# Performance work log

Measured on AMD Instinct MI355X. Metric: run time of the kernel, lower is better.

The kernel has to match this reference:

```python
import jax, jax.numpy as jnp
import numpy as np

H = 16          # n_heads
MAX_REL = 16    # max_relative_position


def _rel_index(S, max_rel):
    # Shaw-style clipped relative-distance index matrix [S, S]
    r = np.arange(S)
    dist = np.clip(r[None, :] - r[:, None], -max_rel, max_rel) + max_rel
    return jnp.asarray(dist, dtype=jnp.int32)


def setup_inputs() -> dict:
    key = jax.random.key(0)
    ks = jax.random.split(key, 16)
    B, S, D = 2, 1024, 1024
    dh = D // H
    n_rel = 2 * MAX_REL + 1
    f = lambda k, shape, scale: (jax.random.normal(k, shape, dtype=jnp.float32) * scale)
    w_scale = 1.0 / np.sqrt(D)
    return {
        "query": f(ks[0], (B, S, D), 1.0),
        "key": f(ks[1], (B, S, D), 1.0),
        "value": f(ks[2], (B, S, D), 1.0),
        "Wq": f(ks[3], (D, D), w_scale), "bq": jnp.zeros((D,), jnp.float32),
        "Wk": f(ks[4], (D, D), w_scale), "bk": jnp.zeros((D,), jnp.float32),
        "Wv": f(ks[5], (D, D), w_scale), "bv": jnp.zeros((D,), jnp.float32),
        "Wo": f(ks[6], (D, D), w_scale), "bo": jnp.zeros((D,), jnp.float32),
        "rel_k": f(ks[7], (n_rel, dh), 1.0 / np.sqrt(dh)),
        "rel_v": f(ks[8], (n_rel, dh), 1.0 / np.sqrt(dh)),
    }


def reference(query, key, value, Wq, bq, Wk, bk, Wv, bv, Wo, bo, rel_k, rel_v):
    B, Sq, D = query.shape
    Sk = key.shape[1]
    dh = D // H
    scale = jnp.sqrt(jnp.asarray(dh, dtype=query.dtype))

    q = (query @ Wq + bq).reshape(B, Sq, H, dh)   # [B,Sq,H,dh]
    k = (key @ Wk + bk).reshape(B, Sk, H, dh)
    v = (value @ Wv + bv).reshape(B, Sk, H, dh)

    idx = _rel_index(max(Sq, Sk), MAX_REL)        # len_q == len_k path
    rk = rel_k[idx]                                # [Sq,Sk,dh]
    rv = rel_v[idx]                                # [Sq,Sk,dh]

    attn1 = jnp.einsum('bqhd,bkhd->bhqk', q, k)
    attn2 = jnp.einsum('bqhd,qkd->bhqk', q, rk)
    attn = jax.nn.softmax((attn1 + attn2) / scale, axis=-1)  # [B,H,Sq,Sk]

    w1 = jnp.einsum('bhqk,bkhd->bhqd', attn, v)
    w2 = jnp.einsum('bhqk,qkd->bhqd', attn, rv)
    x = (w1 + w2).transpose(0, 2, 1, 3).reshape(B, Sq, D)
    return x @ Wo + bo
```

## Files before the change

kernel.cpp:

```cpp
#include <hip/hip_runtime.h>
#include <math.h>

#define Hh 16
#define DH 64
#define NR 33

typedef short s16x8 __attribute__((ext_vector_type(8)));
typedef float f32x4 __attribute__((ext_vector_type(4)));
typedef __fp16 h16x2 __attribute__((ext_vector_type(2)));

static __device__ __forceinline__ short f2h(float f) {
    _Float16 h = (_Float16)f;
    short s; __builtin_memcpy(&s, &h, 2); return s;
}
static __device__ __forceinline__ unsigned pk2h(float a, float b) {
    h16x2 h = __builtin_amdgcn_cvt_pkrtz(a, b);
    unsigned r; __builtin_memcpy(&r, &h, 4); return r;
}

static __device__ __forceinline__ void mfma16(f32x4& c, const s16x8& a, const s16x8& b) {
    asm("s_nop 3\n\tv_mfma_f32_16x16x32_f16 %0, %1, %2, %0"
        : "+v"(c) : "v"(a), "v"(b));
}
static __device__ __forceinline__ void mfma16_last(f32x4& c, const s16x8& a, const s16x8& b) {
    asm("s_nop 3\n\tv_mfma_f32_16x16x32_f16 %0, %1, %2, %0\n\ts_nop 7\n\ts_nop 7"
        : "+v"(c) : "v"(a), "v"(b));
}
static __device__ __forceinline__ void acc_guard(f32x4& c) {
    asm volatile("s_nop 7\n\ts_nop 7" : "+v"(c));
}

static __device__ __forceinline__ void gld16(const short* g, short* l) {
    __builtin_amdgcn_global_load_lds(
        (const __attribute__((address_space(1))) void*)g,
        (__attribute__((address_space(3))) void*)l, 16, 0, 0);
}

static __device__ __forceinline__ s16x8 lds_frag(const short* base, int row, int kb) {
    return *(const s16x8*)((const char*)base + row * 128 + (kb ^ ((row & 7) << 4)));
}

__global__ __launch_bounds__(256)
void cvt_w(const float* __restrict__ W0, const float* __restrict__ W1,
           const float* __restrict__ W2, const float* __restrict__ W3,
           short* __restrict__ Wt) {
    __shared__ float ts[32][33];
    const int z = blockIdx.z;
    const float* W = (z == 0) ? W0 : (z == 1) ? W1 : (z == 2) ? W2 : W3;
    short* O = Wt + (size_t)z * 1024 * 1024;
    const int n0 = blockIdx.x * 32, k0 = blockIdx.y * 32;
    const int tx = threadIdx.x & 31, ty = threadIdx.x >> 5;
    #pragma unroll
    for (int rr = 0; rr < 4; ++rr)
        ts[ty + 8 * rr][tx] = W[(size_t)(k0 + ty + 8 * rr) * 1024 + n0 + tx];
    __syncthreads();
    #pragma unroll
    for (int rr = 0; rr < 4; ++rr)
        O[(size_t)(n0 + ty + 8 * rr) * 1024 + k0 + tx] = f2h(ts[tx][ty + 8 * rr]);
}

__global__ __launch_bounds__(256)
void gemm_qkv(const float* __restrict__ Aq, const float* __restrict__ Ak,
              const float* __restrict__ Av, const short* __restrict__ Wt,
              const float* __restrict__ bq, const float* __restrict__ bk,
              const float* __restrict__ bv, short* __restrict__ Out) {
    __shared__ __align__(16) short As[64 * 64];
    __shared__ __align__(16) short Bs[128 * 64];
    const int tid = threadIdx.x;
    const int wave = tid >> 6, lane = tid & 63;
    const int g = lane >> 4, r = lane & 15;
    const int wm = wave >> 1, wn = wave & 1;
    const int n0 = blockIdx.x * 128;
    const int by = blockIdx.y;
    const int slab = by >> 5;
    const int m0 = (by & 31) * 64;
    const float* A    = (slab == 0) ? Aq : (slab == 1) ? Ak : Av;
    const float* bias = (slab == 0) ? bq : (slab == 1) ? bk : bv;
    const short* Bg = Wt + (size_t)slab * 1024 * 1024;
    short* Og = Out + (size_t)slab * 2048 * 1024;

    const int ar = tid >> 2, ak = tid & 3;
    const float* ap = A + (size_t)(m0 + ar) * 1024 + ak * 16;
    char* asb = (char*)As + ar * 128;
    const int aswz = (ar & 7) << 4;
    const int ao0 = (ak * 32) ^ aswz, ao1 = (ak * 32 + 16) ^ aswz;

    const short* bp[4]; short* bl[4];
    #pragma unroll
    for (int i = 0; i < 4; ++i) {
        int s = i * 256 + tid;
        int row = s >> 3, sk = s & 7;
        int gb = (sk * 16) ^ ((row & 7) << 4);
        bp[i] = Bg + (size_t)(n0 + row) * 1024 + gb / 2;
        bl[i] = Bs + (size_t)(i * 256 + wave * 64) * 8;
    }

    f32x4 acc[2][4] = {};
    #pragma unroll
    for (int mi = 0; mi < 2; ++mi)
        #pragma unroll
        for (int nj = 0; nj < 4; ++nj)
            asm volatile("s_nop 7" : "+v"(acc[mi][nj]));

    for (int kt = 0; kt < 1024; kt += 64) {
        #pragma unroll
        for (int i = 0; i < 4; ++i) gld16(bp[i] + kt, bl[i]);
        float4 va[4];
        #pragma unroll
        for (int c = 0; c < 4; ++c) va[c] = *(const float4*)(ap + kt + c * 4);
        unsigned pk[8];
        #pragma unroll
        for (int c = 0; c < 4; ++c) {
            pk[2 * c]     = pk2h(va[c].x, va[c].y);
            pk[2 * c + 1] = pk2h(va[c].z, va[c].w);
        }
        *(uint4*)(asb + ao0) = *(const uint4*)&pk[0];
        *(uint4*)(asb + ao1) = *(const uint4*)&pk[4];
        asm volatile("s_waitcnt vmcnt(0)" ::: "memory");
        __syncthreads();
        #pragma unroll
        for (int ks = 0; ks < 2; ++ks) {
            s16x8 af[2], bf[4];
            #pragma unroll
            for (int mi = 0; mi < 2; ++mi)
                af[mi] = lds_frag(As, wm * 32 + mi * 16 + r, ks * 64 + g * 16);
            #pragma unroll
            for (int nj = 0; nj < 4; ++nj)
                bf[nj] = lds_frag(Bs, wn * 64 + nj * 16 + r, ks * 64 + g * 16);
            #pragma unroll
            for (int mi = 0; mi < 2; ++mi)
                #pragma unroll
                for (int nj = 0; nj < 4; ++nj)
                    mfma16(acc[mi][nj], af[mi], bf[nj]);
        }
        __syncthreads();
    }
    #pragma unroll
    for (int nj = 0; nj < 4; ++nj) {
        int col = n0 + wn * 64 + nj * 16 + r;
        float bv_ = bias[col];
        #pragma unroll
        for (int mi = 0; mi < 2; ++mi) {
            acc_guard(acc[mi][nj]);
            #pragma unroll
            for (int j = 0; j < 4; ++j) {
                int row = m0 + wm * 32 + mi * 16 + g * 4 + j;
                Og[(size_t)row * 1024 + col] = f2h(acc[mi][nj][j] + bv_);
            }
        }
    }
}

__global__ __launch_bounds__(256)
void gemm_out(const short* __restrict__ Xg, const short* __restrict__ Bg,
              const float* __restrict__ bo, float* __restrict__ Og) {
    __shared__ __align__(16) short As[64 * 64];
    __shared__ __align__(16) short Bs[128 * 64];
    const int tid = threadIdx.x;
    const int wave = tid >> 6, lane = tid & 63;
    const int g = lane >> 4, r = lane & 15;
    const int wm = wave >> 1, wn = wave & 1;
    const int n0 = blockIdx.x * 128;
    const int m0 = blockIdx.y * 64;

    const short* xp[2]; short* xl[2];
    #pragma unroll
    for (int i = 0; i < 2; ++i) {
        int s = i * 256 + tid;
        int row = s >> 3, sk = s & 7;
        int gb = (sk * 16) ^ ((row & 7) << 4);
        xp[i] = Xg + (size_t)(m0 + row) * 1024 + gb / 2;
        xl[i] = As + (size_t)(i * 256 + wave * 64) * 8;
    }
    const short* bp[4]; short* bl[4];
    #pragma unroll
    for (int i = 0; i < 4; ++i) {
        int s = i * 256 + tid;
        int row = s >> 3, sk = s & 7;
        int gb = (sk * 16) ^ ((row & 7) << 4);
        bp[i] = Bg + (size_t)(n0 + row) * 1024 + gb / 2;
        bl[i] = Bs + (size_t)(i * 256 + wave * 64) * 8;
    }

    f32x4 acc[2][4] = {};
    #pragma unroll
    for (int mi = 0; mi < 2; ++mi)
        #pragma unroll
        for (int nj = 0; nj < 4; ++nj)
            asm volatile("s_nop 7" : "+v"(acc[mi][nj]));

    for (int kt = 0; kt < 1024; kt += 64) {
        #pragma unroll
        for (int i = 0; i < 2; ++i) gld16(xp[i] + kt, xl[i]);
        #pragma unroll
        for (int i = 0; i < 4; ++i) gld16(bp[i] + kt, bl[i]);
        asm volatile("s_waitcnt vmcnt(0)" ::: "memory");
        __syncthreads();
        #pragma unroll
        for (int ks = 0; ks < 2; ++ks) {
            s16x8 af[2], bf[4];
            #pragma unroll
            for (int mi = 0; mi < 2; ++mi)
                af[mi] = lds_frag(As, wm * 32 + mi * 16 + r, ks * 64 + g * 16);
            #pragma unroll
            for (int nj = 0; nj < 4; ++nj)
                bf[nj] = lds_frag(Bs, wn * 64 + nj * 16 + r, ks * 64 + g * 16);
            #pragma unroll
            for (int mi = 0; mi < 2; ++mi)
                #pragma unroll
                for (int nj = 0; nj < 4; ++nj)
                    mfma16(acc[mi][nj], af[mi], bf[nj]);
        }
        __syncthreads();
    }
    #pragma unroll
    for (int nj = 0; nj < 4; ++nj) {
        int col = n0 + wn * 64 + nj * 16 + r;
        float bv_ = bo[col];
        #pragma unroll
        for (int mi = 0; mi < 2; ++mi) {
            acc_guard(acc[mi][nj]);
            #pragma unroll
            for (int j = 0; j < 4; ++j) {
                int row = m0 + wm * 32 + mi * 16 + g * 4 + j;
                Og[(size_t)row * 1024 + col] = acc[mi][nj][j] + bv_;
            }
        }
    }
}

#define KSTR 72
#define QRSTR 49
#define RVSTR 68

__global__ __launch_bounds__(256)
void attn_mfma(const short* __restrict__ qg, const short* __restrict__ kg,
               const short* __restrict__ vg, const float* __restrict__ relk,
               const float* __restrict__ relv, short* __restrict__ xg) {
    __shared__ __align__(16) short k_s[64 * KSTR];
    __shared__ __align__(16) short vt_s[64 * KSTR];
    __shared__ __align__(16) short p_s[4][16 * KSTR];
    __shared__ float qr_s[64 * QRSTR];
    __shared__ float W_s[64 * NR];
    __shared__ __align__(16) unsigned char relbuf[NR * RVSTR * 4];

    short* rel_h = (short*)relbuf;
    float* rv_s  = (float*)relbuf;

    const int S = 1024, Dm = 1024;
    const int tid = threadIdx.x;
    const int wave = tid >> 6;
    const int lane = tid & 63;
    const int g = lane >> 4;
    const int r = lane & 15;

    const int blk = blockIdx.x;
    const int bh = blk & 31;
    const int qb = blk >> 5;
    const int b = bh >> 4, h = bh & 15;
    const size_t base = (size_t)b * S * Dm + h * DH;
    const int qw = qb * 64 + wave * 16;

    for (int idx = tid; idx < 48 * 64; idx += 256) {
        int row = idx >> 6, col = idx & 63;
        float val = (row < NR) ? relk[row * 64 + col] : 0.f;
        rel_h[row * KSTR + col] = f2h(val);
    }
    for (int idx = tid; idx < 64 * NR; idx += 256) W_s[idx] = 0.f;
    __syncthreads();

    s16x8 qf[2];
    qf[0] = *(const s16x8*)(qg + base + (size_t)(qw + r) * Dm + g * 8);
    qf[1] = *(const s16x8*)(qg + base + (size_t)(qw + r) * Dm + 32 + g * 8);

    #pragma unroll
    for (int ct = 0; ct < 3; ++ct) {
        f32x4 c = {0.f, 0.f, 0.f, 0.f};
        s16x8 bf0 = *(const s16x8*)&rel_h[(ct * 16 + r) * KSTR + g * 8];
        s16x8 bf1 = *(const s16x8*)&rel_h[(ct * 16 + r) * KSTR + 32 + g * 8];
        mfma16(c, qf[0], bf0);
        mfma16_last(c, qf[1], bf1);
        #pragma unroll
        for (int j = 0; j < 4; ++j)
            qr_s[(wave * 16 + g * 4 + j) * QRSTR + ct * 16 + r] = c[j];
    }

    f32x4 acc[4] = {};
    float l_acc[4] = {0.f, 0.f, 0.f, 0.f};
    float pre[4]   = {0.f, 0.f, 0.f, 0.f};
    float suf[4]   = {0.f, 0.f, 0.f, 0.f};
    const float SCL = 0.18033688f;

    for (int kt = 0; kt < S; kt += 64) {
        __syncthreads();
        #pragma unroll
        for (int i = 0; i < 2; ++i) {
            int idx = tid + 256 * i;
            int row = idx >> 3, c8 = idx & 7;
            s16x8 kv = *(const s16x8*)(kg + base + (size_t)(kt + row) * Dm + c8 * 8);
            s16x8 vv = *(const s16x8*)(vg + base + (size_t)(kt + row) * Dm + c8 * 8);
            *(s16x8*)&k_s[row * KSTR + c8 * 8] = kv;
            #pragma unroll
            for (int e = 0; e < 8; ++e) vt_s[(c8 * 8 + e) * KSTR + row] = vv[e];
        }
        __syncthreads();

        #pragma unroll
        for (int kc = 0; kc < 4; ++kc) {
            f32x4 s = {0.f, 0.f, 0.f, 0.f};
            s16x8 k0 = *(const s16x8*)&k_s[(kc * 16 + r) * KSTR + g * 8];
            s16x8 k1 = *(const s16x8*)&k_s[(kc * 16 + r) * KSTR + 32 + g * 8];
            mfma16(s, qf[0], k0);
            mfma16_last(s, qf[1], k1);
            int k_abs = kt + kc * 16 + r;
            #pragma unroll
            for (int j = 0; j < 4; ++j) {
                int qrow = wave * 16 + g * 4 + j;
                int dist = k_abs - (qb * 64 + qrow);
                int bkt = min(max(dist, -16), 16) + 16;
                float val = (s[j] + qr_s[qrow * QRSTR + bkt]) * SCL;
                float p = exp2f(val);
                l_acc[j] += p;
                if (dist <= -16)      pre[j] += p;
                else if (dist >= 16)  suf[j] += p;
                else                  W_s[qrow * NR + bkt] = p;
                p_s[wave][(g * 4 + j) * KSTR + kc * 16 + r] = f2h(p);
            }
        }

        s16x8 pa0 = *(const s16x8*)&p_s[wave][r * KSTR + g * 8];
        s16x8 pa1 = *(const s16x8*)&p_s[wave][r * KSTR + 32 + g * 8];
        #pragma unroll
        for (int dc = 0; dc < 4; ++dc) {
            s16x8 v0 = *(const s16x8*)&vt_s[(dc * 16 + r) * KSTR + g * 8];
            s16x8 v1 = *(const s16x8*)&vt_s[(dc * 16 + r) * KSTR + 32 + g * 8];
            mfma16(acc[dc], pa0, v0);
            mfma16(acc[dc], pa1, v1);
        }
    }

    #pragma unroll
    for (int j = 0; j < 4; ++j) {
        #pragma unroll
        for (int m = 1; m < 16; m <<= 1) {
            l_acc[j] += __shfl_xor(l_acc[j], m, 16);
            pre[j]   += __shfl_xor(pre[j], m, 16);
            suf[j]   += __shfl_xor(suf[j], m, 16);
        }
    }
    if (r == 0) {
        #pragma unroll
        for (int j = 0; j < 4; ++j) {
            int qrow = wave * 16 + g * 4 + j;
            W_s[qrow * NR + 0]  = pre[j];
            W_s[qrow * NR + 32] = suf[j];
        }
    }

    __syncthreads();
    for (int idx = tid; idx < NR * 64; idx += 256)
        rv_s[(idx >> 6) * RVSTR + (idx & 63)] = relv[idx];
    __syncthreads();

    float R[4][4] = {};
    for (int rr = 0; rr < NR; ++rr) {
        float rvv[4];
        #pragma unroll
        for (int dc = 0; dc < 4; ++dc) rvv[dc] = rv_s[rr * RVSTR + dc * 16 + r];
        #pragma unroll
        for (int j = 0; j < 4; ++j) {
            float w = W_s[(wave * 16 + g * 4 + j) * NR + rr];
            #pragma unroll
            for (int dc = 0; dc < 4; ++dc) R[j][dc] = fmaf(w, rvv[dc], R[j][dc]);
        }
    }
    #pragma unroll
    for (int dc = 0; dc < 4; ++dc) acc_guard(acc[dc]);
    #pragma unroll
    for (int j = 0; j < 4; ++j) {
        float invl = 1.f / l_acc[j];
        size_t o = base + (size_t)(qw + g * 4 + j) * Dm;
        #pragma unroll
        for (int dc = 0; dc < 4; ++dc)
            xg[o + dc * 16 + r] = f2h((acc[dc][j] + R[j][dc]) * invl);
    }
}

extern "C" void kernel_launch(void* const* d_in, const int* in_sizes, int n_in,
                              void* d_out, int out_size, void* d_ws, size_t ws_size,
                              hipStream_t stream) {
    const float* query = (const float*)d_in[0];
    const float* key   = (const float*)d_in[1];
    const float* value = (const float*)d_in[2];
    const float* Wq    = (const float*)d_in[3];
    const float* bq    = (const float*)d_in[4];
    const float* Wk    = (const float*)d_in[5];
    const float* bk    = (const float*)d_in[6];
    const float* Wv    = (const float*)d_in[7];
    const float* bv    = (const float*)d_in[8];
    const float* Wo    = (const float*)d_in[9];
    const float* bo    = (const float*)d_in[10];
    const float* rel_k = (const float*)d_in[11];
    const float* rel_v = (const float*)d_in[12];

    short* wt    = (short*)d_ws;
    short* qkv16 = wt + (size_t)4 * 1024 * 1024;
    short* x16   = qkv16 + (size_t)3 * 2048 * 1024;
    short* q16 = qkv16;
    short* k16 = qkv16 + (size_t)2048 * 1024;
    short* v16 = qkv16 + (size_t)2 * 2048 * 1024;

    cvt_w<<<dim3(32, 32, 4), 256, 0, stream>>>(Wq, Wk, Wv, Wo, wt);
    gemm_qkv<<<dim3(8, 96), 256, 0, stream>>>(query, key, value, wt,
                                              bq, bk, bv, qkv16);
    attn_mfma<<<512, 256, 0, stream>>>(q16, k16, v16, rel_k, rel_v, x16);
    gemm_out<<<dim3(8, 32), 256, 0, stream>>>(x16, wt + (size_t)3 * 1024 * 1024,
                                              bo, (float*)d_out);
}
```

Baseline: 122.0 us.

## Pre-transpose V and load K/V fragments directly from global in attention

Adds a separate kernel that transposes V per head into a [B*H, dh, S] layout. The attention kernel then reads K and V^T MFMA fragments straight from global memory instead of staging them through shared memory, which drops the per-tile __syncthreads and the scalar transpose stores into LDS. It also adds fast paths for key tiles that lie entirely outside the relative-position window, using precomputed clipped biases instead of per-element bucket logic, and it raises the occupancy hint. The cost is an extra kernel launch, the extra global traffic for V^T, and uncoalesced or repeated global fragment loads across waves in place of shared reuse.

```diff
diff --git a/kernel.cpp b/kernel.cpp
--- a/kernel.cpp
+++ b/kernel.cpp
@@ -34,6 +34,9 @@
     __builtin_amdgcn_global_load_lds(
         (const __attribute__((address_space(1))) void*)g,
         (__attribute__((address_space(3))) void*)l, 16, 0, 0);
+}
+static __device__ __forceinline__ void drain_vmem() {
+    asm volatile("s_waitcnt vmcnt(0)" ::: "memory");
 }
 
 static __device__ __forceinline__ s16x8 lds_frag(const short* base, int row, int kb) {
@@ -57,6 +60,33 @@
     #pragma unroll
     for (int rr = 0; rr < 4; ++rr)
         O[(size_t)(n0 + ty + 8 * rr) * 1024 + k0 + tx] = f2h(ts[tx][ty + 8 * rr]);
+}
+
+__global__ __launch_bounds__(256)
+void vT(const short* __restrict__ v16, short* __restrict__ vt16) {
+    __shared__ short ts[64][72];
+    const int st = blockIdx.x;
+    const int bh = blockIdx.y;
+    const int b = bh >> 4, h = bh & 15;
+    const size_t inb = ((size_t)b * 1024 + st * 64) * 1024 + h * 64;
+    #pragma unroll
+    for (int i = 0; i < 2; ++i) {
+        int chunk = i * 256 + threadIdx.x;
+        int row = chunk >> 3, c8 = chunk & 7;
+        *(s16x8*)&ts[row][c8 * 8] =
+            *(const s16x8*)(v16 + inb + (size_t)row * 1024 + c8 * 8);
+    }
+    __syncthreads();
+    const size_t outb = (size_t)(bh * 64) * 1024 + st * 64;
+    #pragma unroll
+    for (int i = 0; i < 2; ++i) {
+        int chunk = i * 256 + threadIdx.x;
+        int d = chunk >> 3, c8 = chunk & 7;
+        s16x8 t;
+        #pragma unroll
+        for (int e = 0; e < 8; ++e) t[e] = ts[c8 * 8 + e][d];
+        *(s16x8*)(vt16 + outb + (size_t)d * 1024 + c8 * 8) = t;
+    }
 }
 
 __global__ __launch_bounds__(256)
@@ -116,7 +146,7 @@
         }
         *(uint4*)(asb + ao0) = *(const uint4*)&pk[0];
         *(uint4*)(asb + ao1) = *(const uint4*)&pk[4];
-        asm volatile("s_waitcnt vmcnt(0)" ::: "memory");
+        drain_vmem();
         __syncthreads();
         #pragma unroll
         for (int ks = 0; ks < 2; ++ks) {
@@ -194,7 +224,7 @@
         for (int i = 0; i < 2; ++i) gld16(xp[i] + kt, xl[i]);
         #pragma unroll
         for (int i = 0; i < 4; ++i) gld16(bp[i] + kt, bl[i]);
-        asm volatile("s_waitcnt vmcnt(0)" ::: "memory");
+        drain_vmem();
         __syncthreads();
         #pragma unroll
         for (int ks = 0; ks < 2; ++ks) {
@@ -229,42 +259,35 @@
     }
 }
 
-#define KSTR 72
 #define QRSTR 49
-#define RVSTR 68
-
-__global__ __launch_bounds__(256)
+
+__global__ __launch_bounds__(256, 3)
 void attn_mfma(const short* __restrict__ qg, const short* __restrict__ kg,
-               const short* __restrict__ vg, const float* __restrict__ relk,
+               const short* __restrict__ vtg, const float* __restrict__ relk,
                const float* __restrict__ relv, short* __restrict__ xg) {
-    __shared__ __align__(16) short k_s[64 * KSTR];
-    __shared__ __align__(16) short vt_s[64 * KSTR];
-    __shared__ __align__(16) short p_s[4][16 * KSTR];
+    __shared__ __align__(16) short p_s[4][16 * 72];
     __shared__ float qr_s[64 * QRSTR];
     __shared__ float W_s[64 * NR];
-    __shared__ __align__(16) unsigned char relbuf[NR * RVSTR * 4];
-
+    __shared__ __align__(16) unsigned char relbuf[8976];
     short* rel_h = (short*)relbuf;
     float* rv_s  = (float*)relbuf;
 
     const int S = 1024, Dm = 1024;
     const int tid = threadIdx.x;
-    const int wave = tid >> 6;
-    const int lane = tid & 63;
-    const int g = lane >> 4;
-    const int r = lane & 15;
-
+    const int wave = tid >> 6, lane = tid & 63;
+    const int g = lane >> 4, r = lane & 15;
     const int blk = blockIdx.x;
     const int bh = blk & 31;
     const int qb = blk >> 5;
     const int b = bh >> 4, h = bh & 15;
     const size_t base = (size_t)b * S * Dm + h * DH;
     const int qw = qb * 64 + wave * 16;
+    const int qs = qb * 64;
 
     for (int idx = tid; idx < 48 * 64; idx += 256) {
         int row = idx >> 6, col = idx & 63;
         float val = (row < NR) ? relk[row * 64 + col] : 0.f;
-        rel_h[row * KSTR + col] = f2h(val);
+        rel_h[row * 72 + col] = f2h(val);
     }
     for (int idx = tid; idx < 64 * NR; idx += 256) W_s[idx] = 0.f;
     __syncthreads();
@@ -276,66 +299,89 @@
     #pragma unroll
     for (int ct = 0; ct < 3; ++ct) {
         f32x4 c = {0.f, 0.f, 0.f, 0.f};
-        s16x8 bf0 = *(const s16x8*)&rel_h[(ct * 16 + r) * KSTR + g * 8];
-        s16x8 bf1 = *(const s16x8*)&rel_h[(ct * 16 + r) * KSTR + 32 + g * 8];
+        s16x8 bf0 = *(const s16x8*)&rel_h[(ct * 16 + r) * 72 + g * 8];
+        s16x8 bf1 = *(const s16x8*)&rel_h[(ct * 16 + r) * 72 + 32 + g * 8];
         mfma16(c, qf[0], bf0);
         mfma16_last(c, qf[1], bf1);
         #pragma unroll
         for (int j = 0; j < 4; ++j)
             qr_s[(wave * 16 + g * 4 + j) * QRSTR + ct * 16 + r] = c[j];
     }
+    __syncthreads();
+
+    float bias0[4], bias32[4];
+    #pragma unroll
+    for (int j = 0; j < 4; ++j) {
+        int qrow = wave * 16 + g * 4 + j;
+        bias0[j]  = qr_s[qrow * QRSTR + 0];
+        bias32[j] = qr_s[qrow * QRSTR + 32];
+    }
 
     f32x4 acc[4] = {};
+    #pragma unroll
+    for (int dc = 0; dc < 4; ++dc)
+        asm volatile("s_nop 7" : "+v"(acc[dc]));
     float l_acc[4] = {0.f, 0.f, 0.f, 0.f};
     float pre[4]   = {0.f, 0.f, 0.f, 0.f};
     float suf[4]   = {0.f, 0.f, 0.f, 0.f};
     const float SCL = 0.18033688f;
+    const short* kbase = kg + base;
+    const short* vbase = vtg + (size_t)(bh * 64) * 1024;
 
     for (int kt = 0; kt < S; kt += 64) {
-        __syncthreads();
-        #pragma unroll
-        for (int i = 0; i < 2; ++i) {
-            int idx = tid + 256 * i;
-            int row = idx >> 3, c8 = idx & 7;
-            s16x8 kv = *(const s16x8*)(kg + base + (size_t)(kt + row) * Dm + c8 * 8);
-            s16x8 vv = *(const s16x8*)(vg + base + (size_t)(kt + row) * Dm + c8 * 8);
-            *(s16x8*)&k_s[row * KSTR + c8 * 8] = kv;
-            #pragma unroll
-            for (int e = 0; e < 8; ++e) vt_s[(c8 * 8 + e) * KSTR + row] = vv[e];
-        }
-        __syncthreads();
-
+        s16x8 vf[4][2];
+        #pragma unroll
+        for (int dc = 0; dc < 4; ++dc)
+            #pragma unroll
+            for (int ks = 0; ks < 2; ++ks)
+                vf[dc][ks] = *(const s16x8*)(vbase + (size_t)(dc * 16 + r) * 1024
+                                             + kt + ks * 32 + g * 8);
+
+        const bool tlo = (kt <= qs - 128), thi = (kt >= qs + 128);
         #pragma unroll
         for (int kc = 0; kc < 4; ++kc) {
+            const short* krow = kbase + (size_t)(kt + kc * 16 + r) * Dm;
+            s16x8 k0 = *(const s16x8*)(krow + g * 8);
+            s16x8 k1 = *(const s16x8*)(krow + 32 + g * 8);
             f32x4 s = {0.f, 0.f, 0.f, 0.f};
-            s16x8 k0 = *(const s16x8*)&k_s[(kc * 16 + r) * KSTR + g * 8];
-            s16x8 k1 = *(const s16x8*)&k_s[(kc * 16 + r) * KSTR + 32 + g * 8];
             mfma16(s, qf[0], k0);
             mfma16_last(s, qf[1], k1);
-            int k_abs = kt + kc * 16 + r;
-            #pragma unroll
-            for (int j = 0; j < 4; ++j) {
-                int qrow = wave * 16 + g * 4 + j;
-                int dist = k_abs - (qb * 64 + qrow);
-                int bkt = min(max(dist, -16), 16) + 16;
-                float val = (s[j] + qr_s[qrow * QRSTR + bkt]) * SCL;
-                float p = exp2f(val);
-                l_acc[j] += p;
-                if (dist <= -16)      pre[j] += p;
-                else if (dist >= 16)  suf[j] += p;
-                else                  W_s[qrow * NR + bkt] = p;
-                p_s[wave][(g * 4 + j) * KSTR + kc * 16 + r] = f2h(p);
+            if (tlo) {
+                #pragma unroll
+                for (int j = 0; j < 4; ++j) {
+                    float p = exp2f((s[j] + bias0[j]) * SCL);
+                    l_acc[j] += p; pre[j] += p;
+                    p_s[wave][(g * 4 + j) * 72 + kc * 16 + r] = f2h(p);
+                }
+            } else if (thi) {
+                #pragma unroll
+                for (int j = 0; j < 4; ++j) {
+                    float p = exp2f((s[j] + bias32[j]) * SCL);
+                    l_acc[j] += p; suf[j] += p;
+                    p_s[wave][(g * 4 + j) * 72 + kc * 16 + r] = f2h(p);
+                }
+            } else {
+                int k_abs = kt + kc * 16 + r;
+                #pragma unroll
+                for (int j = 0; j < 4; ++j) {
+                    int qrow = wave * 16 + g * 4 + j;
+                    int dist = k_abs - (qs + qrow);
+                    int bkt = min(max(dist, -16), 16) + 16;
+                    float p = exp2f((s[j] + qr_s[qrow * QRSTR + bkt]) * SCL);
+                    l_acc[j] += p;
+                    if (dist <= -16)      pre[j] += p;
+                    else if (dist >= 16)  suf[j] += p;
+                    else                  W_s[qrow * NR + bkt] = p;
+                    p_s[wave][(g * 4 + j) * 72 + kc * 16 + r] = f2h(p);
+                }
             }
         }
-
-        s16x8 pa0 = *(const s16x8*)&p_s[wave][r * KSTR + g * 8];
-        s16x8 pa1 = *(const s16x8*)&p_s[wave][r * KSTR + 32 + g * 8];
+        s16x8 pa0 = *(const s16x8*)&p_s[wave][r * 72 + g * 8];
+        s16x8 pa1 = *(const s16x8*)&p_s[wave][r * 72 + 32 + g * 8];
         #pragma unroll
         for (int dc = 0; dc < 4; ++dc) {
-            s16x8 v0 = *(const s16x8*)&vt_s[(dc * 16 + r) * KSTR + g * 8];
-            s16x8 v1 = *(const s16x8*)&vt_s[(dc * 16 + r) * KSTR + 32 + g * 8];
-            mfma16(acc[dc], pa0, v0);
-            mfma16(acc[dc], pa1, v1);
+            mfma16(acc[dc], pa0, vf[dc][0]);
+            mfma16(acc[dc], pa1, vf[dc][1]);
         }
     }
 
@@ -359,14 +405,14 @@
 
     __syncthreads();
     for (int idx = tid; idx < NR * 64; idx += 256)
-        rv_s[(idx >> 6) * RVSTR + (idx & 63)] = relv[idx];
+        rv_s[(idx >> 6) * 68 + (idx & 63)] = relv[idx];
     __syncthreads();
 
     float R[4][4] = {};
     for (int rr = 0; rr < NR; ++rr) {
         float rvv[4];
         #pragma unroll
-        for (int dc = 0; dc < 4; ++dc) rvv[dc] = rv_s[rr * RVSTR + dc * 16 + r];
+        for (int dc = 0; dc < 4; ++dc) rvv[dc] = rv_s[rr * 68 + dc * 16 + r];
         #pragma unroll
         for (int j = 0; j < 4; ++j) {
             float w = W_s[(wave * 16 + g * 4 + j) * NR + rr];
@@ -406,6 +452,7 @@
     short* wt    = (short*)d_ws;
     short* qkv16 = wt + (size_t)4 * 1024 * 1024;
     short* x16   = qkv16 + (size_t)3 * 2048 * 1024;
+    short* vt16  = x16 + (size_t)2048 * 1024;
     short* q16 = qkv16;
     short* k16 = qkv16 + (size_t)2048 * 1024;
     short* v16 = qkv16 + (size_t)2 * 2048 * 1024;
@@ -413,7 +460,8 @@
     cvt_w<<<dim3(32, 32, 4), 256, 0, stream>>>(Wq, Wk, Wv, Wo, wt);
     gemm_qkv<<<dim3(8, 96), 256, 0, stream>>>(query, key, value, wt,
                                               bq, bk, bv, qkv16);
-    attn_mfma<<<512, 256, 0, stream>>>(q16, k16, v16, rel_k, rel_v, x16);
+    vT<<<dim3(16, 32), 256, 0, stream>>>(v16, vt16);
+    attn_mfma<<<512, 256, 0, stream>>>(q16, k16, vt16, rel_k, rel_v, x16);
     gemm_out<<<dim3(8, 32), 256, 0, stream>>>(x16, wt + (size_t)3 * 1024 * 1024,
                                               bo, (float*)d_out);
 }
```

Measured after the change: 135.9 us. 11.3% more time.
